# Performance work log

Measured on AMD Instinct MI355X. Metric: run time of the kernel, lower is better.

## Reference

```python
import jax, jax.numpy as jnp
import numpy as np

N = 100000
E = 3200000
F_IN, F_HID, F_OUT = 512, 16, 40


def setup_inputs() -> dict:
    key = jax.random.key(0)
    k1, k2, k3, k4 = jax.random.split(key, 4)
    x = jax.random.normal(k1, (N, F_IN), dtype=jnp.float32)
    edge_index = jax.random.randint(k2, (2, E), 0, N, dtype=jnp.int64)
    # Glorot-style init for the two GCN layer weights + zero biases
    W1 = jax.random.normal(k3, (F_IN, F_HID), dtype=jnp.float32) / np.sqrt(F_IN)
    b1 = jnp.zeros((F_HID,), dtype=jnp.float32)
    W2 = jax.random.normal(k4, (F_HID, F_OUT), dtype=jnp.float32) / np.sqrt(F_HID)
    b2 = jnp.zeros((F_OUT,), dtype=jnp.float32)
    return {"x": x, "edge_index": edge_index, "W1": W1, "b1": b1, "W2": W2, "b2": b2}


def _gcn_conv(x, src, dst, W, b):
    # x' = D^{-1/2} (A + I) D^{-1/2} (x W) + b   (standard GCNConv with self-loops)
    n = x.shape[0]
    h = x @ W  # [N, F_out] -- transform first (cheap edge traffic)
    deg = jax.ops.segment_sum(jnp.ones_like(dst, dtype=h.dtype), dst, num_segments=n) + 1.0  # +1 self-loop
    dinv = jax.lax.rsqrt(deg)
    msgs = h[src] * (dinv[src] * dinv[dst])[:, None]  # [E, F_out]
    agg = jax.ops.segment_sum(msgs, dst, num_segments=n)
    agg = agg + h * (dinv * dinv)[:, None]  # self-loop contribution
    return agg + b


def reference(x, edge_index, W1, b1, W2, b2):
    src, dst = edge_index[0], edge_index[1]
    h = _gcn_conv(x, src, dst, W1, b1)
    h = jax.nn.relu(h)
    # dropout is identity in eval mode (training=False)
    h = _gcn_conv(h, src, dst, W2, b2)
    return jax.nn.log_softmax(h, axis=1)
```

## Files before the change

kernel.cpp:

```cpp
#include <hip/hip_runtime.h>
#include <hip/hip_fp16.h>
#include <math.h>

#define FIN 512
#define FH 16
#define FOUT 40
#define RANGE 128
#define RSH 7
#define NB_MAX 1024
#define SRC_BITS 17
#define SRC_MASK 0x1FFFF
#define BCHUNK 4096
#define HCHUNK 16384

__global__ __launch_bounds__(256) void histA_k(const int* __restrict__ dst, int E, int NB,
                                               unsigned* __restrict__ bcnt) {
  __shared__ unsigned h[NB_MAX];
  for (int b = threadIdx.x; b < NB; b += 256) h[b] = 0;
  __syncthreads();
  const int base = blockIdx.x * HCHUNK;
  const int cn = min(HCHUNK, E - base);
  for (int u = threadIdx.x; u < cn; u += 256)
    atomicAdd(&h[((unsigned)dst[base + u]) >> RSH], 1u);
  __syncthreads();
  for (int b = threadIdx.x; b < NB; b += 256) {
    unsigned c = h[b];
    if (c) atomicAdd(&bcnt[b], c);
  }
}

__global__ __launch_bounds__(1024) void scanB_k(const unsigned* __restrict__ bcnt, int NB,
                                                unsigned* __restrict__ boff,
                                                unsigned* __restrict__ bcur) {
  __shared__ unsigned ws[16];
  const int t = threadIdx.x, lane = t & 63, wid = t >> 6;
  unsigned v = (t < NB) ? bcnt[t] : 0;
  unsigned incl = v;
#pragma unroll
  for (int d = 1; d < 64; d <<= 1) {
    unsigned o = __shfl_up(incl, d);
    if (lane >= d) incl += o;
  }
  if (lane == 63) ws[wid] = incl;
  __syncthreads();
  unsigned woff = 0, tot = 0;
#pragma unroll
  for (int w = 0; w < 16; ++w) {
    unsigned s = ws[w];
    if (w < wid) woff += s;
    tot += s;
  }
  unsigned ex = woff + incl - v;
  if (t < NB) { boff[t] = ex; bcur[t] = ex; }
  if (t == 0) boff[NB] = tot;
}

__global__ __launch_bounds__(256) void bin_k(const int* __restrict__ src,
                                             const int* __restrict__ dst, int E, int NB,
                                             unsigned* __restrict__ bcur,
                                             unsigned* __restrict__ bins) {
  __shared__ unsigned hist[NB_MAX];
  __shared__ unsigned excl[NB_MAX];
  __shared__ unsigned gbase[NB_MAX];
  __shared__ unsigned lcur[NB_MAX];
  __shared__ unsigned stage[BCHUNK];
  __shared__ unsigned short sbkt[BCHUNK];
  __shared__ unsigned wtot[4];
  const int t = threadIdx.x, lane = t & 63, wid = t >> 6;
  for (int b = t; b < NB; b += 256) hist[b] = 0;
  __syncthreads();
  const int base = blockIdx.x * BCHUNK;
  const int cn = min(BCHUNK, E - base);
  for (int u = t; u < cn; u += 256)
    atomicAdd(&hist[((unsigned)dst[base + u]) >> RSH], 1u);
  __syncthreads();
  unsigned loc[4], s = 0;
#pragma unroll
  for (int j = 0; j < 4; ++j) {
    int idx = t * 4 + j;
    loc[j] = s;
    s += (idx < NB) ? hist[idx] : 0;
  }
  unsigned incl = s;
#pragma unroll
  for (int d = 1; d < 64; d <<= 1) {
    unsigned o = __shfl_up(incl, d);
    if (lane >= d) incl += o;
  }
  if (lane == 63) wtot[wid] = incl;
  __syncthreads();
  unsigned woff = 0;
  for (int w = 0; w < wid; ++w) woff += wtot[w];
  unsigned tex = woff + incl - s;
#pragma unroll
  for (int j = 0; j < 4; ++j) {
    int idx = t * 4 + j;
    if (idx < NB) excl[idx] = tex + loc[j];
  }
  __syncthreads();
  for (int b = t; b < NB; b += 256) {
    unsigned c = hist[b];
    gbase[b] = c ? atomicAdd(&bcur[b], c) : 0u;
    lcur[b] = excl[b];
  }
  __syncthreads();
  for (int u = t; u < cn; u += 256) {
    int e = base + u;
    unsigned d = (unsigned)dst[e];
    unsigned bkt = d >> RSH;
    unsigned pk = ((unsigned)src[e]) | ((d & (RANGE - 1)) << SRC_BITS);
    unsigned lr = atomicAdd(&lcur[bkt], 1u);
    stage[lr] = pk;
    sbkt[lr] = (unsigned short)bkt;
  }
  __syncthreads();
  for (int u = t; u < cn; u += 256) {
    unsigned bkt = sbkt[u];
    bins[gbase[bkt] + (u - excl[bkt])] = stage[u];
  }
}

__global__ __launch_bounds__(256) void deg_k(const unsigned* __restrict__ boff,
                                             const unsigned* __restrict__ bins, int n,
                                             float* __restrict__ dinv) {
  __shared__ unsigned dh[RANGE];
  const int t = threadIdx.x, b = blockIdx.x;
  if (t < RANGE) dh[t] = 0;
  __syncthreads();
  const unsigned jb = boff[b], je = boff[b + 1];
  for (unsigned j = jb + t; j < je; j += 256) atomicAdd(&dh[bins[j] >> SRC_BITS], 1u);
  __syncthreads();
  const int i = b * RANGE + t;
  if (t < RANGE && i < n) dinv[i] = rsqrtf((float)dh[t] + 1.0f);
}

__global__ __launch_bounds__(256) void gemm1_k(const float* __restrict__ x,
                                               const float* __restrict__ W1,
                                               const float* __restrict__ dinv, int n,
                                               __half* __restrict__ hs1) {
  __shared__ float w1s[FIN * FH];
  for (int idx = threadIdx.x; idx < FIN * FH; idx += 256) w1s[idx] = W1[idx];
  __syncthreads();

  const int row_raw = blockIdx.x * 256 + threadIdx.x;
  const int row = row_raw < n ? row_raw : n - 1;
  const float4* __restrict__ xr = (const float4*)(x + (size_t)row * FIN);

  float4 a0 = {0, 0, 0, 0}, a1 = {0, 0, 0, 0}, a2 = {0, 0, 0, 0}, a3 = {0, 0, 0, 0};

#pragma unroll 2
  for (int it = 0; it < FIN / 4; ++it) {
    float4 xv = xr[it];
    const float* wf = w1s + it * 4 * FH;
#pragma unroll
    for (int j = 0; j < 4; ++j) {
      const float xj = (j == 0) ? xv.x : (j == 1) ? xv.y : (j == 2) ? xv.z : xv.w;
      const float* wj = wf + j * FH;
      float4 w0 = *(const float4*)(wj + 0);
      float4 w1 = *(const float4*)(wj + 4);
      float4 w2 = *(const float4*)(wj + 8);
      float4 w3 = *(const float4*)(wj + 12);
      a0.x += xj * w0.x; a0.y += xj * w0.y; a0.z += xj * w0.z; a0.w += xj * w0.w;
      a1.x += xj * w1.x; a1.y += xj * w1.y; a1.z += xj * w1.z; a1.w += xj * w1.w;
      a2.x += xj * w2.x; a2.y += xj * w2.y; a2.z += xj * w2.z; a2.w += xj * w2.w;
      a3.x += xj * w3.x; a3.y += xj * w3.y; a3.z += xj * w3.z; a3.w += xj * w3.w;
    }
  }

  if (row_raw < n) {
    const float di = dinv[row];
    __half2 hb[8];
    hb[0] = __floats2half2_rn(a0.x * di, a0.y * di);
    hb[1] = __floats2half2_rn(a0.z * di, a0.w * di);
    hb[2] = __floats2half2_rn(a1.x * di, a1.y * di);
    hb[3] = __floats2half2_rn(a1.z * di, a1.w * di);
    hb[4] = __floats2half2_rn(a2.x * di, a2.y * di);
    hb[5] = __floats2half2_rn(a2.z * di, a2.w * di);
    hb[6] = __floats2half2_rn(a3.x * di, a3.y * di);
    hb[7] = __floats2half2_rn(a3.z * di, a3.w * di);
    uint4* o = (uint4*)(hs1 + (size_t)row * FH);
    o[0] = ((const uint4*)hb)[0];
    o[1] = ((const uint4*)hb)[1];
  }
}

__global__ __launch_bounds__(512) void gather1_k(const __half* __restrict__ hs1,
                                                 const unsigned* __restrict__ boff,
                                                 const unsigned* __restrict__ bins,
                                                 const float* __restrict__ dinv,
                                                 const float* __restrict__ b1, int n,
                                                 __half* __restrict__ rs) {
  __shared__ float acc[RANGE * FH];
  __shared__ float b1s[FH];
  const int t = threadIdx.x, b = blockIdx.x;
  if (t < FH) b1s[t] = b1[t];
  for (int u = t; u < RANGE * FH; u += 512) acc[u] = 0.f;
  __syncthreads();
  const unsigned jb = boff[b], je = boff[b + 1];
  const int k = t & 15, slot = t >> 4;
  unsigned j = jb + slot;
  for (; j + 96 < je; j += 128) {
    const unsigned p0 = bins[j];
    const unsigned p1 = bins[j + 32];
    const unsigned p2 = bins[j + 64];
    const unsigned p3 = bins[j + 96];
    const float v0 = __half2float(hs1[(size_t)(p0 & SRC_MASK) * FH + k]);
    const float v1 = __half2float(hs1[(size_t)(p1 & SRC_MASK) * FH + k]);
    const float v2 = __half2float(hs1[(size_t)(p2 & SRC_MASK) * FH + k]);
    const float v3 = __half2float(hs1[(size_t)(p3 & SRC_MASK) * FH + k]);
    atomicAdd(&acc[(p0 >> SRC_BITS) * FH + k], v0);
    atomicAdd(&acc[(p1 >> SRC_BITS) * FH + k], v1);
    atomicAdd(&acc[(p2 >> SRC_BITS) * FH + k], v2);
    atomicAdd(&acc[(p3 >> SRC_BITS) * FH + k], v3);
  }
  for (; j < je; j += 32) {
    const unsigned p = bins[j];
    atomicAdd(&acc[(p >> SRC_BITS) * FH + k],
              __half2float(hs1[(size_t)(p & SRC_MASK) * FH + k]));
  }
  __syncthreads();
  const int base = b * RANGE;
  const float4* acc4 = (const float4*)acc;
  {
    const int fi = t;
    const int node = fi >> 2, sub = fi & 3;
    const int i = base + node;
    if (i < n) {
      const float4 a = acc4[fi];
      const __half2* hp = (const __half2*)(hs1 + (size_t)i * FH + sub * 4);
      const float2 h0 = __half22float2(hp[0]);
      const float2 h1 = __half22float2(hp[1]);
      const float d = dinv[i];
      float r0 = (a.x + h0.x) * d + b1s[sub * 4 + 0];
      float r1 = (a.y + h0.y) * d + b1s[sub * 4 + 1];
      float r2 = (a.z + h1.x) * d + b1s[sub * 4 + 2];
      float r3 = (a.w + h1.y) * d + b1s[sub * 4 + 3];
      r0 = fmaxf(r0, 0.f) * d;
      r1 = fmaxf(r1, 0.f) * d;
      r2 = fmaxf(r2, 0.f) * d;
      r3 = fmaxf(r3, 0.f) * d;
      __half2* rp = (__half2*)(rs + (size_t)i * FH + sub * 4);
      rp[0] = __floats2half2_rn(r0, r1);
      rp[1] = __floats2half2_rn(r2, r3);
    }
  }
}

__global__ __launch_bounds__(512) void gather2_k(const __half* __restrict__ rs,
                                                 const unsigned* __restrict__ boff,
                                                 const unsigned* __restrict__ bins,
                                                 const float* __restrict__ dinv,
                                                 const float* __restrict__ W2,
                                                 const float* __restrict__ b2, int n,
                                                 float* __restrict__ out) {
  __shared__ float acc[RANGE * FH];
  __shared__ float w2s[FH * FOUT + FOUT];
  const int t = threadIdx.x, b = blockIdx.x;
  for (int idx = t; idx < FH * FOUT + FOUT; idx += 512)
    w2s[idx] = (idx < FH * FOUT) ? W2[idx] : b2[idx - FH * FOUT];
  for (int u = t; u < RANGE * FH; u += 512) acc[u] = 0.f;
  __syncthreads();
  const unsigned jb = boff[b], je = boff[b + 1];
  const int k = t & 15, slot = t >> 4;
  unsigned j = jb + slot;
  for (; j + 96 < je; j += 128) {
    const unsigned p0 = bins[j];
    const unsigned p1 = bins[j + 32];
    const unsigned p2 = bins[j + 64];
    const unsigned p3 = bins[j + 96];
    const float v0 = __half2float(rs[(size_t)(p0 & SRC_MASK) * FH + k]);
    const float v1 = __half2float(rs[(size_t)(p1 & SRC_MASK) * FH + k]);
    const float v2 = __half2float(rs[(size_t)(p2 & SRC_MASK) * FH + k]);
    const float v3 = __half2float(rs[(size_t)(p3 & SRC_MASK) * FH + k]);
    atomicAdd(&acc[(p0 >> SRC_BITS) * FH + k], v0);
    atomicAdd(&acc[(p1 >> SRC_BITS) * FH + k], v1);
    atomicAdd(&acc[(p2 >> SRC_BITS) * FH + k], v2);
    atomicAdd(&acc[(p3 >> SRC_BITS) * FH + k], v3);
  }
  for (; j < je; j += 32) {
    const unsigned p = bins[j];
    atomicAdd(&acc[(p >> SRC_BITS) * FH + k],
              __half2float(rs[(size_t)(p & SRC_MASK) * FH + k]));
  }
  __syncthreads();
  const int base = b * RANGE;
  float4* acc4 = (float4*)acc;
  {
    const int fi = t;
    const int node = fi >> 2, sub = fi & 3;
    const int i = base + node;
    if (i < n) {
      float4 a = acc4[fi];
      const __half2* rp = (const __half2*)(rs + (size_t)i * FH + sub * 4);
      const float2 r0 = __half22float2(rp[0]);
      const float2 r1 = __half22float2(rp[1]);
      const float d = dinv[i];
      a.x = (a.x + r0.x) * d;
      a.y = (a.y + r0.y) * d;
      a.z = (a.z + r1.x) * d;
      a.w = (a.w + r1.y) * d;
      acc4[fi] = a;
    }
  }
  __syncthreads();
  const int lane = t & 63, wv = t >> 6;
  for (int nd = wv; nd < RANGE; nd += 8) {
    const int i = base + nd;
    if (i >= n) continue;
    float hv = (lane < FOUT) ? w2s[FH * FOUT + lane] : 0.f;
#pragma unroll
    for (int kk = 0; kk < 16; ++kk) {
      const float a = acc[nd * FH + kk];
      if (lane < FOUT) hv += a * w2s[kk * FOUT + lane];
    }
    float m = (lane < FOUT) ? hv : -INFINITY;
#pragma unroll
    for (int d = 1; d < 64; d <<= 1) m = fmaxf(m, __shfl_xor(m, d));
    float ex = (lane < FOUT) ? expf(hv - m) : 0.f;
#pragma unroll
    for (int d = 1; d < 64; d <<= 1) ex += __shfl_xor(ex, d);
    if (lane < FOUT) out[(size_t)i * FOUT + lane] = hv - m - logf(ex);
  }
}

extern "C" void kernel_launch(void* const* d_in, const int* in_sizes, int n_in,
                              void* d_out, int out_size, void* d_ws, size_t ws_size,
                              hipStream_t stream) {
  const float* x  = (const float*)d_in[0];
  const int*   ei = (const int*)d_in[1];
  const float* W1 = (const float*)d_in[2];
  const float* b1 = (const float*)d_in[3];
  const float* W2 = (const float*)d_in[4];
  const float* b2 = (const float*)d_in[5];
  float* out = (float*)d_out;

  const int n = in_sizes[0] / FIN;
  const int E = in_sizes[1] / 2;
  const int* src = ei;
  const int* dst = ei + E;
  const int NB = (n + RANGE - 1) >> RSH;

  char* ws = (char*)d_ws;
  size_t o = 0;
  auto alloc = [&](size_t bytes) {
    void* p = ws + o;
    o = (o + bytes + 255) & ~(size_t)255;
    return p;
  };
  unsigned* bcnt = (unsigned*)alloc((size_t)(NB + 1) * 4);
  unsigned* boff = (unsigned*)alloc((size_t)(NB + 1) * 4);
  unsigned* bcur = (unsigned*)alloc((size_t)NB * 4);
  float*    dinv = (float*)alloc((size_t)n * 4);
  unsigned* bins = (unsigned*)alloc((size_t)E * 4);
  __half*   hs1  = (__half*)alloc((size_t)n * FH * 2);
  __half*   rsb  = (__half*)alloc((size_t)n * FH * 2);

  hipMemsetAsync(bcnt, 0, (size_t)(NB + 1) * 4, stream);

  histA_k<<<(E + HCHUNK - 1) / HCHUNK, 256, 0, stream>>>(dst, E, NB, bcnt);
  scanB_k<<<1, 1024, 0, stream>>>(bcnt, NB, boff, bcur);
  bin_k<<<(E + BCHUNK - 1) / BCHUNK, 256, 0, stream>>>(src, dst, E, NB, bcur, bins);
  deg_k<<<NB, 256, 0, stream>>>(boff, bins, n, dinv);

  gemm1_k<<<(n + 255) / 256, 256, 0, stream>>>(x, W1, dinv, n, hs1);
  gather1_k<<<NB, 512, 0, stream>>>(hs1, boff, bins, dinv, b1, n, rsb);
  gather2_k<<<NB, 512, 0, stream>>>(rsb, boff, bins, dinv, W2, b2, n, out);
}
```

Before: 855.1 us.

## Process one edge per thread with vector row loads and padded LDS accumulators

The gather kernels switch from 16 threads per edge, each loading a single half feature, to one thread per edge that loads the full 32-byte source row with two uint4 loads and performs 16 LDS atomic adds. The accumulator rows are padded to 17 floats so that different destinations touching the same feature land in different LDS banks, and the next packed edge is prefetched one step ahead. The goal is fewer global load instructions and more edges in flight per wave. The cost is a more scattered access pattern per lane, more registers, and serial atomics within each thread.

```diff
diff --git a/kernel.cpp b/kernel.cpp
--- a/kernel.cpp
+++ b/kernel.cpp
@@ -12,6 +12,7 @@
 #define SRC_MASK 0x1FFFF
 #define BCHUNK 4096
 #define HCHUNK 16384
+#define AP 17
 
 __global__ __launch_bounds__(256) void histA_k(const int* __restrict__ dst, int E, int NB,
                                                unsigned* __restrict__ bcnt) {
@@ -184,57 +185,62 @@
   }
 }
 
+__device__ __forceinline__ void edge_accum(const __half* __restrict__ tab,
+                                           unsigned pk, float* __restrict__ acc) {
+  const int s = pk & SRC_MASK;
+  const int dl = pk >> SRC_BITS;
+  const uint4* rp = (const uint4*)(tab + (size_t)s * FH);
+  const uint4 q0 = rp[0];
+  const uint4 q1 = rp[1];
+  float* arow = acc + dl * AP;
+  float2 f;
+  f = __half22float2(*(const __half2*)&q0.x); atomicAdd(arow + 0, f.x);  atomicAdd(arow + 1, f.y);
+  f = __half22float2(*(const __half2*)&q0.y); atomicAdd(arow + 2, f.x);  atomicAdd(arow + 3, f.y);
+  f = __half22float2(*(const __half2*)&q0.z); atomicAdd(arow + 4, f.x);  atomicAdd(arow + 5, f.y);
+  f = __half22float2(*(const __half2*)&q0.w); atomicAdd(arow + 6, f.x);  atomicAdd(arow + 7, f.y);
+  f = __half22float2(*(const __half2*)&q1.x); atomicAdd(arow + 8, f.x);  atomicAdd(arow + 9, f.y);
+  f = __half22float2(*(const __half2*)&q1.y); atomicAdd(arow + 10, f.x); atomicAdd(arow + 11, f.y);
+  f = __half22float2(*(const __half2*)&q1.z); atomicAdd(arow + 12, f.x); atomicAdd(arow + 13, f.y);
+  f = __half22float2(*(const __half2*)&q1.w); atomicAdd(arow + 14, f.x); atomicAdd(arow + 15, f.y);
+}
+
 __global__ __launch_bounds__(512) void gather1_k(const __half* __restrict__ hs1,
                                                  const unsigned* __restrict__ boff,
                                                  const unsigned* __restrict__ bins,
                                                  const float* __restrict__ dinv,
                                                  const float* __restrict__ b1, int n,
                                                  __half* __restrict__ rs) {
-  __shared__ float acc[RANGE * FH];
+  __shared__ float acc[RANGE * AP];
   __shared__ float b1s[FH];
   const int t = threadIdx.x, b = blockIdx.x;
   if (t < FH) b1s[t] = b1[t];
-  for (int u = t; u < RANGE * FH; u += 512) acc[u] = 0.f;
+  for (int u = t; u < RANGE * AP; u += 512) acc[u] = 0.f;
   __syncthreads();
   const unsigned jb = boff[b], je = boff[b + 1];
-  const int k = t & 15, slot = t >> 4;
-  unsigned j = jb + slot;
-  for (; j + 96 < je; j += 128) {
-    const unsigned p0 = bins[j];
-    const unsigned p1 = bins[j + 32];
-    const unsigned p2 = bins[j + 64];
-    const unsigned p3 = bins[j + 96];
-    const float v0 = __half2float(hs1[(size_t)(p0 & SRC_MASK) * FH + k]);
-    const float v1 = __half2float(hs1[(size_t)(p1 & SRC_MASK) * FH + k]);
-    const float v2 = __half2float(hs1[(size_t)(p2 & SRC_MASK) * FH + k]);
-    const float v3 = __half2float(hs1[(size_t)(p3 & SRC_MASK) * FH + k]);
-    atomicAdd(&acc[(p0 >> SRC_BITS) * FH + k], v0);
-    atomicAdd(&acc[(p1 >> SRC_BITS) * FH + k], v1);
-    atomicAdd(&acc[(p2 >> SRC_BITS) * FH + k], v2);
-    atomicAdd(&acc[(p3 >> SRC_BITS) * FH + k], v3);
-  }
-  for (; j < je; j += 32) {
-    const unsigned p = bins[j];
-    atomicAdd(&acc[(p >> SRC_BITS) * FH + k],
-              __half2float(hs1[(size_t)(p & SRC_MASK) * FH + k]));
+  unsigned j = jb + t;
+  unsigned pk = (j < je) ? bins[j] : 0u;
+  while (j < je) {
+    const unsigned j2 = j + 512;
+    const unsigned pk2 = (j2 < je) ? bins[j2] : 0u;
+    edge_accum(hs1, pk, acc);
+    j = j2; pk = pk2;
   }
   __syncthreads();
   const int base = b * RANGE;
-  const float4* acc4 = (const float4*)acc;
   {
-    const int fi = t;
-    const int node = fi >> 2, sub = fi & 3;
+    const int node = t >> 2, sub = t & 3;
     const int i = base + node;
     if (i < n) {
-      const float4 a = acc4[fi];
+      const float* arow = acc + node * AP + sub * 4;
+      const float a0 = arow[0], a1 = arow[1], a2 = arow[2], a3 = arow[3];
       const __half2* hp = (const __half2*)(hs1 + (size_t)i * FH + sub * 4);
       const float2 h0 = __half22float2(hp[0]);
       const float2 h1 = __half22float2(hp[1]);
       const float d = dinv[i];
-      float r0 = (a.x + h0.x) * d + b1s[sub * 4 + 0];
-      float r1 = (a.y + h0.y) * d + b1s[sub * 4 + 1];
-      float r2 = (a.z + h1.x) * d + b1s[sub * 4 + 2];
-      float r3 = (a.w + h1.y) * d + b1s[sub * 4 + 3];
+      float r0 = (a0 + h0.x) * d + b1s[sub * 4 + 0];
+      float r1 = (a1 + h0.y) * d + b1s[sub * 4 + 1];
+      float r2 = (a2 + h1.x) * d + b1s[sub * 4 + 2];
+      float r3 = (a3 + h1.y) * d + b1s[sub * 4 + 3];
       r0 = fmaxf(r0, 0.f) * d;
       r1 = fmaxf(r1, 0.f) * d;
       r2 = fmaxf(r2, 0.f) * d;
@@ -253,53 +259,37 @@
                                                  const float* __restrict__ W2,
                                                  const float* __restrict__ b2, int n,
                                                  float* __restrict__ out) {
-  __shared__ float acc[RANGE * FH];
+  __shared__ float acc[RANGE * AP];
   __shared__ float w2s[FH * FOUT + FOUT];
   const int t = threadIdx.x, b = blockIdx.x;
   for (int idx = t; idx < FH * FOUT + FOUT; idx += 512)
     w2s[idx] = (idx < FH * FOUT) ? W2[idx] : b2[idx - FH * FOUT];
-  for (int u = t; u < RANGE * FH; u += 512) acc[u] = 0.f;
+  for (int u = t; u < RANGE * AP; u += 512) acc[u] = 0.f;
   __syncthreads();
   const unsigned jb = boff[b], je = boff[b + 1];
-  const int k = t & 15, slot = t >> 4;
-  unsigned j = jb + slot;
-  for (; j + 96 < je; j += 128) {
-    const unsigned p0 = bins[j];
-    const unsigned p1 = bins[j + 32];
-    const unsigned p2 = bins[j + 64];
-    const unsigned p3 = bins[j + 96];
-    const float v0 = __half2float(rs[(size_t)(p0 & SRC_MASK) * FH + k]);
-    const float v1 = __half2float(rs[(size_t)(p1 & SRC_MASK) * FH + k]);
-    const float v2 = __half2float(rs[(size_t)(p2 & SRC_MASK) * FH + k]);
-    const float v3 = __half2float(rs[(size_t)(p3 & SRC_MASK) * FH + k]);
-    atomicAdd(&acc[(p0 >> SRC_BITS) * FH + k], v0);
-    atomicAdd(&acc[(p1 >> SRC_BITS) * FH + k], v1);
-    atomicAdd(&acc[(p2 >> SRC_BITS) * FH + k], v2);
-    atomicAdd(&acc[(p3 >> SRC_BITS) * FH + k], v3);
-  }
-  for (; j < je; j += 32) {
-    const unsigned p = bins[j];
-    atomicAdd(&acc[(p >> SRC_BITS) * FH + k],
-              __half2float(rs[(size_t)(p & SRC_MASK) * FH + k]));
+  unsigned j = jb + t;
+  unsigned pk = (j < je) ? bins[j] : 0u;
+  while (j < je) {
+    const unsigned j2 = j + 512;
+    const unsigned pk2 = (j2 < je) ? bins[j2] : 0u;
+    edge_accum(rs, pk, acc);
+    j = j2; pk = pk2;
   }
   __syncthreads();
   const int base = b * RANGE;
-  float4* acc4 = (float4*)acc;
   {
-    const int fi = t;
-    const int node = fi >> 2, sub = fi & 3;
+    const int node = t >> 2, sub = t & 3;
     const int i = base + node;
     if (i < n) {
-      float4 a = acc4[fi];
+      float* arow = acc + node * AP + sub * 4;
       const __half2* rp = (const __half2*)(rs + (size_t)i * FH + sub * 4);
       const float2 r0 = __half22float2(rp[0]);
       const float2 r1 = __half22float2(rp[1]);
       const float d = dinv[i];
-      a.x = (a.x + r0.x) * d;
-      a.y = (a.y + r0.y) * d;
-      a.z = (a.z + r1.x) * d;
-      a.w = (a.w + r1.y) * d;
-      acc4[fi] = a;
+      arow[0] = (arow[0] + r0.x) * d;
+      arow[1] = (arow[1] + r0.y) * d;
+      arow[2] = (arow[2] + r1.x) * d;
+      arow[3] = (arow[3] + r1.y) * d;
     }
   }
   __syncthreads();
@@ -310,7 +300,7 @@
     float hv = (lane < FOUT) ? w2s[FH * FOUT + lane] : 0.f;
 #pragma unroll
     for (int kk = 0; kk < 16; ++kk) {
-      const float a = acc[nd * FH + kk];
+      const float a = acc[nd * AP + kk];
       if (lane < FOUT) hv += a * w2s[kk * FOUT + lane];
     }
     float m = (lane < FOUT) ? hv : -INFINITY;
```

After: 873.0 us. 1.02x slower.
